# Performance work log

Measured on AMD Instinct MI355X. Metric: run time of the kernel, lower is better.

## Reference

```python
import jax, jax.numpy as jnp
import numpy as np

T, B, I, H = 1024, 64, 512, 512


def setup_inputs() -> dict:
    key = jax.random.key(0)
    ks = jax.random.split(key, 7)
    s_in = 1.0 / np.sqrt(H)
    return {
        "input": jax.random.normal(ks[0], (T, B, I), jnp.float32),
        "h0": jax.random.normal(ks[1], (B, H), jnp.float32),
        "c0": jax.random.normal(ks[2], (B, H), jnp.float32),
        "W_ih": jax.random.normal(ks[3], (4 * H, I), jnp.float32) * s_in,
        "W_hh": jax.random.normal(ks[4], (4 * H, H), jnp.float32) * s_in,
        "b_ih": jax.random.normal(ks[5], (4 * H,), jnp.float32) * s_in,
        "b_hh": jax.random.normal(ks[6], (4 * H,), jnp.float32) * s_in,
    }


def reference(input, h0, c0, W_ih, W_hh, b_ih, b_hh):
    # Precompute input projections for all timesteps in one big GEMM: [T,B,4H]
    x_proj = jnp.einsum('tbi,gi->tbg', input, W_ih) + b_ih + b_hh

    def step(carry, x_p):
        h, c = carry
        gates = jax.nn.sigmoid(x_p + h @ W_hh.T)  # [B,4H], all gates sigmoid (subLSTM)
        i, f, z, o = jnp.split(gates, 4, axis=-1)
        c_new = f * c + z - i
        h_new = jax.nn.sigmoid(c_new) - o
        return (h_new, c_new), h_new

    # reverse=True == torch code: reverse inputs, scan, reverse outputs back
    (h_f, c_f), outputs = jax.lax.scan(step, (h0, c0), x_proj, reverse=True)
    return outputs, (h_f, c_f)
```

## Files before the change

### kernel.cpp

```cpp
#include <hip/hip_runtime.h>
#include <hip/hip_bf16.h>

typedef float  f32x2  __attribute__((ext_vector_type(2)));
typedef float  f32x4  __attribute__((ext_vector_type(4)));
typedef float  f32x16 __attribute__((ext_vector_type(16)));
typedef __bf16 bfrag8 __attribute__((ext_vector_type(8)));
typedef __bf16 bf16x4 __attribute__((ext_vector_type(4)));

#define T_STEPS 1024
#define BB 64
#define II 512
#define HH 512
#define G4 2048
#define NB 64
#define BH (BB*HH)

static __device__ inline unsigned short bf16_bits(float f) {
  union { __bf16 h; unsigned short u; } v; v.h = (__bf16)f; return v.u;
}
static __device__ inline float sigm(float x) { return 1.f / (1.f + __expf(-x)); }

__global__ void k_init_h(const float* __restrict__ h0, unsigned* __restrict__ hb) {
  int i = blockIdx.x * 256 + threadIdx.x;
  if (i < BH) hb[i] = ((unsigned)bf16_bits(h0[i]) << 16);
  else        hb[i] = 0x0000FFFFu;
}

template<bool XF32>
__global__ __launch_bounds__(256) void k_xproj(
    const float* __restrict__ inp, const float* __restrict__ Wih,
    const float* __restrict__ bih, const float* __restrict__ bhh,
    void* __restrict__ xp_) {
  constexpr int BM = 128, BN = 128, BK = 64, LDK = 72;
  __shared__ __bf16 As[BM][LDK];
  __shared__ __bf16 Bs[BN][LDK];
  const int bx = blockIdx.x;
  const int tm = bx >> 4, tn = bx & 15;
  const int m0 = tm * BM, n0 = tn * BN;
  const int tid = threadIdx.x;
  const int lane = tid & 63, w = tid >> 6;
  const int wm = w >> 1, wn = w & 1;
  const int l31 = lane & 31, lhi = lane >> 5;

  f32x16 acc[2][2] = {};

  const int srow = tid >> 2;
  const int sq = tid & 3;

  for (int k0 = 0; k0 < 512; k0 += BK) {
    __syncthreads();
    #pragma unroll
    for (int j = 0; j < 2; j++) {
      const int r = srow + 64 * j;
      const float* pa = inp + (size_t)(m0 + r) * II + k0 + sq * 16;
      const float* pb = Wih + (size_t)(n0 + r) * II + k0 + sq * 16;
      #pragma unroll
      for (int i = 0; i < 4; i++) {
        f32x4 va = *(const f32x4*)(pa + 4 * i);
        bf16x4 wa; wa[0]=(__bf16)va[0]; wa[1]=(__bf16)va[1]; wa[2]=(__bf16)va[2]; wa[3]=(__bf16)va[3];
        *(bf16x4*)&As[r][sq * 16 + 4 * i] = wa;
        f32x4 vb = *(const f32x4*)(pb + 4 * i);
        bf16x4 wb; wb[0]=(__bf16)vb[0]; wb[1]=(__bf16)vb[1]; wb[2]=(__bf16)vb[2]; wb[3]=(__bf16)vb[3];
        *(bf16x4*)&Bs[r][sq * 16 + 4 * i] = wb;
      }
    }
    __syncthreads();
    #pragma unroll
    for (int ks = 0; ks < 4; ks++) {
      const int kk = ks * 16 + 8 * lhi;
      bfrag8 af0 = *(const bfrag8*)&As[64 * wm +      l31][kk];
      bfrag8 af1 = *(const bfrag8*)&As[64 * wm + 32 + l31][kk];
      bfrag8 bf0 = *(const bfrag8*)&Bs[64 * wn +      l31][kk];
      bfrag8 bf1 = *(const bfrag8*)&Bs[64 * wn + 32 + l31][kk];
      acc[0][0] = __builtin_amdgcn_mfma_f32_32x32x16_bf16(af0, bf0, acc[0][0], 0, 0, 0);
      acc[0][1] = __builtin_amdgcn_mfma_f32_32x32x16_bf16(af0, bf1, acc[0][1], 0, 0, 0);
      acc[1][0] = __builtin_amdgcn_mfma_f32_32x32x16_bf16(af1, bf0, acc[1][0], 0, 0, 0);
      acc[1][1] = __builtin_amdgcn_mfma_f32_32x32x16_bf16(af1, bf1, acc[1][1], 0, 0, 0);
    }
  }
  #pragma unroll
  for (int a = 0; a < 2; a++)
    #pragma unroll
    for (int b = 0; b < 2; b++) {
      const int col = n0 + 64 * wn + 32 * b + l31;
      const float bias = bih[col] + bhh[col];
      #pragma unroll
      for (int q = 0; q < 16; q++) {
        const int row = m0 + 64 * wm + 32 * a + (q & 3) + 8 * (q >> 2) + 4 * lhi;
        const float v = acc[a][b][q] + bias;
        if constexpr (XF32) ((float*)xp_)[(size_t)row * G4 + col] = v;
        else                ((__bf16*)xp_)[(size_t)row * G4 + col] = (__bf16)v;
      }
    }
}

template<bool XF32>
__global__ __launch_bounds__(256, 1) void k_recur(
    const float* __restrict__ Whh, const float* __restrict__ c0,
    const void* __restrict__ xp_, unsigned* __restrict__ hb,
    float* __restrict__ out) {
  const int bid = blockIdx.x;
  const int rb = bid & 1;
  const int g  = bid >> 1;
  const int tid = threadIdx.x;
  const int lane = tid & 63, w = tid >> 6;
  const int tt = w & 1, kh = w >> 1;
  const int l31 = lane & 31, lhi = lane >> 5;

  __shared__ __bf16 hA[32][520];
  __shared__ float pS[2][2][32][33];

  const int gate = tt * 2 + (l31 >> 4);
  const int gcol = gate * 512 + g * 16 + (l31 & 15);

  bfrag8 bw[16];
  #pragma unroll
  for (int ks = 0; ks < 16; ks++) {
    const float* p = Whh + (size_t)gcol * HH + kh * 256 + ks * 16 + 8 * lhi;
    f32x4 v0 = *(const f32x4*)p;
    f32x4 v1 = *(const f32x4*)(p + 4);
    bfrag8 f;
    f[0]=(__bf16)v0[0]; f[1]=(__bf16)v0[1]; f[2]=(__bf16)v0[2]; f[3]=(__bf16)v0[3];
    f[4]=(__bf16)v1[0]; f[5]=(__bf16)v1[1]; f[6]=(__bf16)v1[2]; f[7]=(__bf16)v1[3];
    bw[ks] = f;
  }

  const int lb = tid >> 3, c2 = (tid & 7) * 2;
  const int brow = 32 * rb + lb;
  const int jcol = 16 * g + c2;
  f32x2 creg = *(const f32x2*)(c0 + (size_t)brow * HH + jcol);

  const int str = w * 8 + (lane >> 3);
  const int sb  = lane & 7;

  int xrow[16];
  #pragma unroll
  for (int q = 0; q < 16; q++) xrow[q] = (q & 3) + 8 * (q >> 2) + 4 * lhi;

  f32x16 xv_cur = {}, xv_nxt = {};
  if (kh == 0) {
    #pragma unroll
    for (int q = 0; q < 16; q++) {
      const size_t idx = ((size_t)(T_STEPS - 1) * BB + 32 * rb + xrow[q]) * G4 + gcol;
      if constexpr (XF32) xv_cur[q] = ((const float*)xp_)[idx];
      else                xv_cur[q] = (float)((const __bf16*)xp_)[idx];
    }
  }

  for (int s = 0; s < T_STEPS; s++) {
    const int t = T_STEPS - 1 - s;

    const unsigned long long* hrow = (const unsigned long long*)
        (hb + (size_t)(s & 1) * BH + (size_t)(32 * rb + str) * HH);
    const unsigned long long tpat = 0x0000FFFF0000FFFFull;
    const unsigned long long texp = (unsigned long long)s * 0x0000000100000001ull;
    unsigned long long v[32];
    unsigned need = 0xFFFFFFFFu;
    for (;;) {
      #pragma unroll
      for (int i = 0; i < 32; i++)
        if (need & (1u << i))
          v[i] = __hip_atomic_load(hrow + sb + 8 * i,
                                   __ATOMIC_RELAXED, __HIP_MEMORY_SCOPE_AGENT);
      unsigned miss = 0;
      #pragma unroll
      for (int i = 0; i < 32; i++)
        if ((need & (1u << i)) && ((v[i] & tpat) != texp)) miss |= 1u << i;
      if (miss == 0) break;
      need = miss;
    }
    #pragma unroll
    for (int i = 0; i < 32; i++) {
      const unsigned lo = (unsigned)v[i], hi = (unsigned)(v[i] >> 32);
      const unsigned packed = (lo >> 16) | (hi & 0xFFFF0000u);
      *(unsigned*)&hA[str][(sb + 8 * i) * 2] = packed;
    }

    if (kh == 0 && s + 1 < T_STEPS) {
      #pragma unroll
      for (int q = 0; q < 16; q++) {
        const size_t idx = ((size_t)(t - 1) * BB + 32 * rb + xrow[q]) * G4 + gcol;
        if constexpr (XF32) xv_nxt[q] = ((const float*)xp_)[idx];
        else                xv_nxt[q] = (float)((const __bf16*)xp_)[idx];
      }
    }
    __syncthreads();

    f32x16 acc = {};
    #pragma unroll
    for (int ks = 0; ks < 16; ks++) {
      bfrag8 a = *(const bfrag8*)&hA[l31][kh * 256 + ks * 16 + 8 * lhi];
      acc = __builtin_amdgcn_mfma_f32_32x32x16_bf16(a, bw[ks], acc, 0, 0, 0);
    }
    #pragma unroll
    for (int q = 0; q < 16; q++) {
      const int row = (q & 3) + 8 * (q >> 2) + 4 * lhi;
      pS[kh][tt][row][l31] = (kh == 0) ? (acc[q] + xv_cur[q]) : acc[q];
    }
    __syncthreads();

    {
      float sg[4][2];
      #pragma unroll
      for (int gt = 0; gt < 4; gt++) {
        const int tl = gt >> 1, off = (gt & 1) * 16;
        #pragma unroll
        for (int dc = 0; dc < 2; dc++) {
          const int col = off + c2 + dc;
          sg[gt][dc] = sigm(pS[0][tl][lb][col] + pS[1][tl][lb][col]);
        }
      }
      const float cn0 = sg[1][0] * creg[0] + sg[2][0] - sg[0][0];
      const float cn1 = sg[1][1] * creg[1] + sg[2][1] - sg[0][1];
      creg[0] = cn0; creg[1] = cn1;
      const float hn0 = sigm(cn0) - sg[3][0];
      const float hn1 = sigm(cn1) - sg[3][1];
      const unsigned tag = (unsigned)(s + 1);
      const unsigned plo = ((unsigned)bf16_bits(hn0) << 16) | tag;
      const unsigned phi = ((unsigned)bf16_bits(hn1) << 16) | tag;
      const unsigned long long pv = ((unsigned long long)phi << 32) | plo;
      __hip_atomic_store((unsigned long long*)
          (hb + (size_t)((s + 1) & 1) * BH + (size_t)brow * HH + jcol),
          pv, __ATOMIC_RELAXED, __HIP_MEMORY_SCOPE_AGENT);
      f32x2 hv; hv[0] = hn0; hv[1] = hn1;
      __builtin_nontemporal_store(hv,
          (f32x2*)(out + (size_t)t * BH + (size_t)brow * HH + jcol));
      if (s == T_STEPS - 1) {
        f32x2 cv; cv[0] = cn0; cv[1] = cn1;
        *(f32x2*)(out + (size_t)T_STEPS * BH + (size_t)brow * HH + jcol) = hv;
        *(f32x2*)(out + (size_t)T_STEPS * BH + BH + (size_t)brow * HH + jcol) = cv;
      }
    }
    xv_cur = xv_nxt;
  }
}

extern "C" void kernel_launch(void* const* d_in, const int* in_sizes, int n_in,
                              void* d_out, int out_size, void* d_ws, size_t ws_size,
                              hipStream_t stream) {
  (void)in_sizes; (void)n_in; (void)out_size;
  const float* inp = (const float*)d_in[0];
  const float* h0  = (const float*)d_in[1];
  const float* c0  = (const float*)d_in[2];
  const float* Wih = (const float*)d_in[3];
  const float* Whh = (const float*)d_in[4];
  const float* bih = (const float*)d_in[5];
  const float* bhh = (const float*)d_in[6];
  float* out = (float*)d_out;
  char* ws = (char*)d_ws;

  unsigned* hb = (unsigned*)ws;
  void*     xp = (void*)(ws + (1u << 20));
  const size_t need_f32 = (1u << 20) + (size_t)T_STEPS * BB * G4 * 4;
  const bool xf32 = ws_size >= need_f32;

  k_init_h<<<2 * BH / 256, 256, 0, stream>>>(h0, hb);
  const int gemm_grid = (T_STEPS * BB / 128) * (G4 / 128);
  if (xf32) {
    k_xproj<true ><<<gemm_grid, 256, 0, stream>>>(inp, Wih, bih, bhh, xp);
    k_recur<true ><<<NB, 256, 0, stream>>>(Whh, c0, xp, hb, out);
  } else {
    k_xproj<false><<<gemm_grid, 256, 0, stream>>>(inp, Wih, bih, bhh, xp);
    k_recur<false><<<NB, 256, 0, stream>>>(Whh, c0, xp, hb, out);
  }
}
```

Before: 5.400 ms.

## Replace per-element tagged h exchange with per-block stamp flags and packed bf16

The recurrent kernel stops embedding a step tag in every hidden-state element, where each consumer polled all 32 words per row. Instead it stores plain packed bf16 h values and has each block publish a per-block step counter after a vmcnt wait and barrier. One wavefront spins on the 32 producer stamps it depends on. The h rows are then read with cache-bypassing dwordx4 loads, which halves the exchanged bytes and the number of polled loads. The design relies on the data stores becoming visible before the relaxed stamp store, with only a waitcnt and no release fence, so there is a memory-ordering risk.

```diff
diff --git a/kernel.cpp b/kernel.cpp
--- a/kernel.cpp
+++ b/kernel.cpp
@@ -6,6 +6,7 @@
 typedef float  f32x16 __attribute__((ext_vector_type(16)));
 typedef __bf16 bfrag8 __attribute__((ext_vector_type(8)));
 typedef __bf16 bf16x4 __attribute__((ext_vector_type(4)));
+typedef int    i32x4  __attribute__((ext_vector_type(4)));
 
 #define T_STEPS 1024
 #define BB 64
@@ -20,10 +21,11 @@
 }
 static __device__ inline float sigm(float x) { return 1.f / (1.f + __expf(-x)); }
 
-__global__ void k_init_h(const float* __restrict__ h0, unsigned* __restrict__ hb) {
+__global__ void k_init_h(const float* __restrict__ h0, __bf16* __restrict__ hb,
+                         unsigned* __restrict__ stamps) {
   int i = blockIdx.x * 256 + threadIdx.x;
-  if (i < BH) hb[i] = ((unsigned)bf16_bits(h0[i]) << 16);
-  else        hb[i] = 0x0000FFFFu;
+  hb[i] = (__bf16)h0[i];
+  if (blockIdx.x == 0 && threadIdx.x < NB) stamps[threadIdx.x] = 0u;
 }
 
 template<bool XF32>
@@ -43,7 +45,6 @@
   const int l31 = lane & 31, lhi = lane >> 5;
 
   f32x16 acc[2][2] = {};
-
   const int srow = tid >> 2;
   const int sq = tid & 3;
 
@@ -97,8 +98,8 @@
 template<bool XF32>
 __global__ __launch_bounds__(256, 1) void k_recur(
     const float* __restrict__ Whh, const float* __restrict__ c0,
-    const void* __restrict__ xp_, unsigned* __restrict__ hb,
-    float* __restrict__ out) {
+    const void* __restrict__ xp_, __bf16* __restrict__ hb,
+    unsigned* __restrict__ stamps, float* __restrict__ out) {
   const int bid = blockIdx.x;
   const int rb = bid & 1;
   const int g  = bid >> 1;
@@ -147,34 +148,36 @@
     }
   }
 
+  const unsigned* mystamp = stamps + 2 * l31 + rb;
+
   for (int s = 0; s < T_STEPS; s++) {
     const int t = T_STEPS - 1 - s;
 
-    const unsigned long long* hrow = (const unsigned long long*)
-        (hb + (size_t)(s & 1) * BH + (size_t)(32 * rb + str) * HH);
-    const unsigned long long tpat = 0x0000FFFF0000FFFFull;
-    const unsigned long long texp = (unsigned long long)s * 0x0000000100000001ull;
-    unsigned long long v[32];
-    unsigned need = 0xFFFFFFFFu;
-    for (;;) {
-      #pragma unroll
-      for (int i = 0; i < 32; i++)
-        if (need & (1u << i))
-          v[i] = __hip_atomic_load(hrow + sb + 8 * i,
-                                   __ATOMIC_RELAXED, __HIP_MEMORY_SCOPE_AGENT);
-      unsigned miss = 0;
-      #pragma unroll
-      for (int i = 0; i < 32; i++)
-        if ((need & (1u << i)) && ((v[i] & tpat) != texp)) miss |= 1u << i;
-      if (miss == 0) break;
-      need = miss;
-    }
-    #pragma unroll
-    for (int i = 0; i < 32; i++) {
-      const unsigned lo = (unsigned)v[i], hi = (unsigned)(v[i] >> 32);
-      const unsigned packed = (lo >> 16) | (hi & 0xFFFF0000u);
-      *(unsigned*)&hA[str][(sb + 8 * i) * 2] = packed;
-    }
+    if (w == 0 && s > 0) {
+      for (;;) {
+        unsigned st = (lane < 32)
+            ? __hip_atomic_load(mystamp, __ATOMIC_RELAXED, __HIP_MEMORY_SCOPE_AGENT)
+            : 0xFFFFFFFFu;
+        if (__all((int)(st >= (unsigned)s))) break;
+      }
+    }
+    __builtin_amdgcn_s_barrier();
+    asm volatile("" ::: "memory");
+
+    const char* hbase = (const char*)hb
+        + (size_t)(s & 1) * (BH * 2)
+        + ((size_t)(32 * rb + str) * HH + sb * 8) * 2;
+    i32x4 hv[8];
+    #pragma unroll
+    for (int i = 0; i < 8; i++) {
+      unsigned long long a64 = (unsigned long long)(hbase + i * 128);
+      asm volatile("global_load_dwordx4 %0, %1, off sc0 sc1"
+                   : "=v"(hv[i]) : "v"(a64));
+    }
+    asm volatile("s_waitcnt vmcnt(0)" ::: "memory");
+    #pragma unroll
+    for (int i = 0; i < 8; i++)
+      *(i32x4*)&hA[str][sb * 8 + i * 64] = hv[i];
 
     if (kh == 0 && s + 1 < T_STEPS) {
       #pragma unroll
@@ -184,9 +187,13 @@
         else                xv_nxt[q] = (float)((const __bf16*)xp_)[idx];
       }
     }
-    __syncthreads();
-
-    f32x16 acc = {};
+    asm volatile("s_waitcnt lgkmcnt(0)" ::: "memory");
+    __builtin_amdgcn_s_barrier();
+    asm volatile("" ::: "memory");
+
+    f32x16 acc;
+    #pragma unroll
+    for (int q = 0; q < 16; q++) acc[q] = (kh == 0) ? xv_cur[q] : 0.f;
     #pragma unroll
     for (int ks = 0; ks < 16; ks++) {
       bfrag8 a = *(const bfrag8*)&hA[l31][kh * 256 + ks * 16 + 8 * lhi];
@@ -195,10 +202,13 @@
     #pragma unroll
     for (int q = 0; q < 16; q++) {
       const int row = (q & 3) + 8 * (q >> 2) + 4 * lhi;
-      pS[kh][tt][row][l31] = (kh == 0) ? (acc[q] + xv_cur[q]) : acc[q];
-    }
-    __syncthreads();
-
+      pS[kh][tt][row][l31] = acc[q];
+    }
+    asm volatile("s_waitcnt lgkmcnt(0)" ::: "memory");
+    __builtin_amdgcn_s_barrier();
+    asm volatile("" ::: "memory");
+
+    float cn0, cn1, hn0, hn1;
     {
       float sg[4][2];
       #pragma unroll
@@ -210,26 +220,30 @@
           sg[gt][dc] = sigm(pS[0][tl][lb][col] + pS[1][tl][lb][col]);
         }
       }
-      const float cn0 = sg[1][0] * creg[0] + sg[2][0] - sg[0][0];
-      const float cn1 = sg[1][1] * creg[1] + sg[2][1] - sg[0][1];
+      cn0 = sg[1][0] * creg[0] + sg[2][0] - sg[0][0];
+      cn1 = sg[1][1] * creg[1] + sg[2][1] - sg[0][1];
       creg[0] = cn0; creg[1] = cn1;
-      const float hn0 = sigm(cn0) - sg[3][0];
-      const float hn1 = sigm(cn1) - sg[3][1];
-      const unsigned tag = (unsigned)(s + 1);
-      const unsigned plo = ((unsigned)bf16_bits(hn0) << 16) | tag;
-      const unsigned phi = ((unsigned)bf16_bits(hn1) << 16) | tag;
-      const unsigned long long pv = ((unsigned long long)phi << 32) | plo;
-      __hip_atomic_store((unsigned long long*)
+      hn0 = sigm(cn0) - sg[3][0];
+      hn1 = sigm(cn1) - sg[3][1];
+      const unsigned pk = ((unsigned)bf16_bits(hn0)) | ((unsigned)bf16_bits(hn1) << 16);
+      __hip_atomic_store((unsigned*)
           (hb + (size_t)((s + 1) & 1) * BH + (size_t)brow * HH + jcol),
-          pv, __ATOMIC_RELAXED, __HIP_MEMORY_SCOPE_AGENT);
-      f32x2 hv; hv[0] = hn0; hv[1] = hn1;
-      __builtin_nontemporal_store(hv,
-          (f32x2*)(out + (size_t)t * BH + (size_t)brow * HH + jcol));
-      if (s == T_STEPS - 1) {
-        f32x2 cv; cv[0] = cn0; cv[1] = cn1;
-        *(f32x2*)(out + (size_t)T_STEPS * BH + (size_t)brow * HH + jcol) = hv;
-        *(f32x2*)(out + (size_t)T_STEPS * BH + BH + (size_t)brow * HH + jcol) = cv;
-      }
+          pk, __ATOMIC_RELAXED, __HIP_MEMORY_SCOPE_AGENT);
+    }
+    asm volatile("s_waitcnt vmcnt(0)" ::: "memory");
+    __builtin_amdgcn_s_barrier();
+    asm volatile("" ::: "memory");
+    if (tid == 0)
+      __hip_atomic_store(stamps + bid, (unsigned)(s + 1),
+                         __ATOMIC_RELAXED, __HIP_MEMORY_SCOPE_AGENT);
+
+    f32x2 hvv; hvv[0] = hn0; hvv[1] = hn1;
+    __builtin_nontemporal_store(hvv,
+        (f32x2*)(out + (size_t)t * BH + (size_t)brow * HH + jcol));
+    if (s == T_STEPS - 1) {
+      f32x2 cv; cv[0] = cn0; cv[1] = cn1;
+      *(f32x2*)(out + (size_t)T_STEPS * BH + (size_t)brow * HH + jcol) = hvv;
+      *(f32x2*)(out + (size_t)T_STEPS * BH + BH + (size_t)brow * HH + jcol) = cv;
     }
     xv_cur = xv_nxt;
   }
@@ -249,18 +263,19 @@
   float* out = (float*)d_out;
   char* ws = (char*)d_ws;
 
-  unsigned* hb = (unsigned*)ws;
-  void*     xp = (void*)(ws + (1u << 20));
+  unsigned* stamps = (unsigned*)ws;
+  __bf16*   hb     = (__bf16*)(ws + 4096);
+  void*     xp     = (void*)(ws + (1u << 20));
   const size_t need_f32 = (1u << 20) + (size_t)T_STEPS * BB * G4 * 4;
   const bool xf32 = ws_size >= need_f32;
 
-  k_init_h<<<2 * BH / 256, 256, 0, stream>>>(h0, hb);
+  k_init_h<<<BH / 256, 256, 0, stream>>>(h0, hb, stamps);
   const int gemm_grid = (T_STEPS * BB / 128) * (G4 / 128);
   if (xf32) {
     k_xproj<true ><<<gemm_grid, 256, 0, stream>>>(inp, Wih, bih, bhh, xp);
-    k_recur<true ><<<NB, 256, 0, stream>>>(Whh, c0, xp, hb, out);
+    k_recur<true ><<<NB, 256, 0, stream>>>(Whh, c0, xp, hb, stamps, out);
   } else {
     k_xproj<false><<<gemm_grid, 256, 0, stream>>>(inp, Wih, bih, bhh, xp);
-    k_recur<false><<<NB, 256, 0, stream>>>(Whh, c0, xp, hb, out);
-  }
-}
+    k_recur<false><<<NB, 256, 0, stream>>>(Whh, c0, xp, hb, stamps, out);
+  }
+}
```

Result: faster. 4.710 ms (-12.8%).
